# Kernel tuning notes

Measured on AMD Instinct MI355X. Metric: run time of the kernel, lower is better.

Reference implementation:

```python
import jax, jax.numpy as jnp
import numpy as np

D_MODEL = 1024
N_HEADS = 16
D_HEAD = D_MODEL // N_HEADS
D_FF = 4096
BATCH = 2
SEQ = 2048
LN_EPS = 1e-5


def setup_inputs() -> dict:
    key = jax.random.key(0)
    ks = jax.random.split(key, 12)
    s = 1.0 / np.sqrt(D_MODEL)
    x = jax.random.normal(ks[0], (BATCH, SEQ, D_MODEL), dtype=jnp.float32)
    mask = jnp.broadcast_to(jnp.tril(jnp.ones((SEQ, SEQ), jnp.int32)), (BATCH, SEQ, SEQ))
    return {
        "x": x,
        "mask": mask,
        # per-head projections stacked: [H, D, Dh] (bias=False in source)
        "Wq": jax.random.normal(ks[1], (N_HEADS, D_MODEL, D_HEAD), jnp.float32) * s,
        "Wk": jax.random.normal(ks[2], (N_HEADS, D_MODEL, D_HEAD), jnp.float32) * s,
        "Wv": jax.random.normal(ks[3], (N_HEADS, D_MODEL, D_HEAD), jnp.float32) * s,
        "Wo": jax.random.normal(ks[4], (D_MODEL, D_MODEL), jnp.float32) * s,
        "ln1_w": jnp.ones((D_MODEL,), jnp.float32),
        "ln1_b": jnp.zeros((D_MODEL,), jnp.float32),
        "ln2_w": jnp.ones((D_MODEL,), jnp.float32),
        "ln2_b": jnp.zeros((D_MODEL,), jnp.float32),
        "W1": jax.random.normal(ks[5], (D_MODEL, D_FF), jnp.float32) * s,
        "b1": jnp.zeros((D_FF,), jnp.float32),
        "W2": jax.random.normal(ks[6], (D_FF, D_MODEL), jnp.float32) * (1.0 / np.sqrt(D_FF)),
        "b2": jnp.zeros((D_MODEL,), jnp.float32),
    }


def layer_norm(x, w, b):
    mu = jnp.mean(x, axis=-1, keepdims=True)
    var = jnp.var(x, axis=-1, keepdims=True)
    return (x - mu) * jax.lax.rsqrt(var + LN_EPS) * w + b


def reference(x, mask, Wq, Wk, Wv, Wo, ln1_w, ln1_b, ln2_w, ln2_b, W1, b1, W2, b2):
    # pre-LN masked self-attention
    h = layer_norm(x, ln1_w, ln1_b)
    q = jnp.einsum("bsd,hde->bhse", h, Wq)  # [B,H,S,Dh]
    k = jnp.einsum("bsd,hde->bhse", h, Wk)
    v = jnp.einsum("bsd,hde->bhse", h, Wv)
    scores = jnp.einsum("bhse,bhte->bhst", q, k) / np.sqrt(D_HEAD)
    scores = jnp.where(mask[:, None, :, :].astype(bool), scores, -jnp.inf)
    weights = jax.nn.softmax(scores, axis=-1)
    attn = jnp.einsum("bhst,bhte->bhse", weights, v)  # [B,H,S,Dh]
    # concat heads (head order = last-dim order in torch.cat)
    concat = attn.transpose(0, 2, 1, 3).reshape(x.shape[0], x.shape[1], D_MODEL)
    att_out = concat @ Wo
    att_x = x + att_out
    # FFN with exact (erf) GELU, matching nn.GELU default
    h2 = layer_norm(att_x, ln2_w, ln2_b)
    ff = jax.nn.gelu(h2 @ W1 + b1, approximate=False) @ W2 + b2
    return att_x + ff
```

## Files before the change

kernel.cpp:

```cpp
#include <hip/hip_runtime.h>
#include <hip/hip_bf16.h>
#include <math.h>

#define D_MODEL 1024
#define N_HEADS 16
#define D_HEAD  64
#define D_FF    4096
#define BATCH   2
#define SEQ     2048
#define NTOK    (BATCH*SEQ)

typedef __hip_bfloat16 bf16;
typedef __attribute__((ext_vector_type(8))) short short8;
typedef __attribute__((ext_vector_type(4))) float floatx4;

template<typename TIN>
__global__ void ln_kernel(const TIN* __restrict__ x,
                          const float* __restrict__ w,
                          const float* __restrict__ b,
                          bf16* __restrict__ out) {
    int row = blockIdx.x;
    int tid = threadIdx.x;
    const long base = (long)row * D_MODEL;
    float v[4];
    float s = 0.f, sq = 0.f;
#pragma unroll
    for (int i = 0; i < 4; ++i) {
        float xv = (float)x[base + tid + i*256];
        v[i] = xv; s += xv; sq += xv*xv;
    }
    __shared__ float r1[256], r2[256];
    r1[tid] = s; r2[tid] = sq; __syncthreads();
    for (int off = 128; off > 0; off >>= 1) {
        if (tid < off) { r1[tid] += r1[tid+off]; r2[tid] += r2[tid+off]; }
        __syncthreads();
    }
    float mean = r1[0] * (1.f/D_MODEL);
    float var  = r2[0] * (1.f/D_MODEL) - mean*mean;
    float rstd = rsqrtf(var + 1e-5f);
#pragma unroll
    for (int i = 0; i < 4; ++i) {
        int c = tid + i*256;
        out[base + c] = __float2bfloat16((v[i] - mean) * rstd * w[c] + b[c]);
    }
}

__global__ __launch_bounds__(256) void wcvt_kernel(const float* __restrict__ W,
                                                   bf16* __restrict__ Wt,
                                                   int K, int N) {
    __shared__ float t[32][33];
    int n0 = blockIdx.x * 32, k0 = blockIdx.y * 32;
    int lx = threadIdx.x & 31, ly = threadIdx.x >> 5;
#pragma unroll
    for (int i = 0; i < 4; ++i) {
        int k = ly + i * 8;
        t[k][lx] = W[(long)(k0 + k) * N + n0 + lx];
    }
    __syncthreads();
#pragma unroll
    for (int i = 0; i < 4; ++i) {
        int n = ly + i * 8;
        Wt[(long)(n0 + n) * K + k0 + lx] = __float2bfloat16(t[lx][n]);
    }
}

__global__ __launch_bounds__(256) void wcvt_wo_w1(const float* __restrict__ Wo,
                                                  const float* __restrict__ W1,
                                                  bf16* __restrict__ wo_bf,
                                                  bf16* __restrict__ w1_bf) {
    __shared__ float t[32][33];
    int gx = blockIdx.x;
    const float* W; bf16* Wt; int N, n0;
    if (gx < 32) { W = Wo; Wt = wo_bf; N = D_MODEL; n0 = gx * 32; }
    else         { W = W1; Wt = w1_bf; N = D_FF;    n0 = (gx - 32) * 32; }
    int k0 = blockIdx.y * 32;
    int lx = threadIdx.x & 31, ly = threadIdx.x >> 5;
#pragma unroll
    for (int i = 0; i < 4; ++i) {
        int k = ly + i * 8;
        t[k][lx] = W[(long)(k0 + k) * N + n0 + lx];
    }
    __syncthreads();
#pragma unroll
    for (int i = 0; i < 4; ++i) {
        int n = ly + i * 8;
        Wt[(long)(n0 + n) * D_MODEL + k0 + lx] = __float2bfloat16(t[lx][n]);
    }
}

__global__ __launch_bounds__(256) void wcvt_qkv(const float* __restrict__ Wq,
                                                const float* __restrict__ Wk,
                                                const float* __restrict__ Wv,
                                                bf16* __restrict__ outp) {
    __shared__ float t[32][33];
    int z = blockIdx.z, mat = z >> 4, head = z & 15;
    const float* W = (mat == 0 ? Wq : mat == 1 ? Wk : Wv) + (long)head * D_MODEL * D_HEAD;
    bf16* Wt = outp + (long)z * D_HEAD * D_MODEL;
    int n0 = blockIdx.x * 32, k0 = blockIdx.y * 32;
    int lx = threadIdx.x & 31, ly = threadIdx.x >> 5;
#pragma unroll
    for (int i = 0; i < 4; ++i) {
        int k = ly + i * 8;
        t[k][lx] = W[(long)(k0 + k) * D_HEAD + n0 + lx];
    }
    __syncthreads();
#pragma unroll
    for (int i = 0; i < 4; ++i) {
        int n = ly + i * 8;
        Wt[(long)(n0 + n) * D_MODEL + k0 + lx] = __float2bfloat16(t[lx][n]);
    }
}

__device__ inline void swz2d(int& bx, int& by) {
    int gx = gridDim.x;
    int nwg = gx * gridDim.y;
    int bid = blockIdx.y * gx + blockIdx.x;
    int swz = (bid & 7) * (nwg >> 3) + (bid >> 3);
    bx = swz % gx;
    by = swz / gx;
}

template<int ROWS>
__device__ inline void stage_tile(const bf16* g, int gstride, short* lds) {
    int lane = threadIdx.x & 63, wave = threadIdx.x >> 6;
#pragma unroll
    for (int it = 0; it < ROWS / 64; ++it) {
        int c = wave + it * 4;
        const bf16* gp = g + (long)(c * 16 + (lane >> 2)) * gstride + (lane & 3) * 8;
        short* lp = lds + c * 512 + lane * 8;
        __builtin_amdgcn_global_load_lds(
            (const __attribute__((address_space(1))) void*)gp,
            (__attribute__((address_space(3))) void*)lp, 16, 0, 0);
    }
}

template<int BM, int BN, int BK>
__device__ inline void gemm_accum(const bf16* __restrict__ A, int lda,
                                  const bf16* __restrict__ Wt, int K,
                                  int row0, int col0, short* As, short* Bs,
                                  floatx4 (&acc)[BM/32][BN/32]) {
    constexpr int MI  = BM / 32;
    constexpr int NR  = BN / 32;
    constexpr int ASZ = BM * BK;
    constexpr int BSZ = BN * BK;
    int tid  = threadIdx.x;
    int wave = tid >> 6, lane = tid & 63;
    int quad = lane >> 4, l16 = lane & 15;
    int wm = (wave >> 1) * (BM / 2);
    int wn = (wave & 1) * (BN / 2);

    auto stage = [&](int k0, int buf) {
#pragma unroll
        for (int kk = 0; kk < BK; kk += 32) {
            stage_tile<BM>(A  + (long)row0 * lda + k0 + kk, lda,
                           As + buf * ASZ + (kk / 32) * BM * 32);
            stage_tile<BN>(Wt + (long)col0 * K   + k0 + kk, K,
                           Bs + buf * BSZ + (kk / 32) * BN * 32);
        }
    };

    stage(0, 0);
    __syncthreads();

    int cur = 0;
    for (int k0 = 0; k0 < K; k0 += BK) {
        if (k0 + BK < K) stage(k0 + BK, cur ^ 1);

#pragma unroll
        for (int p = 0; p < BK / 32; ++p) {
            const short* Ap = As + cur * ASZ + p * BM * 32;
            const short* Bp = Bs + cur * BSZ + p * BN * 32;
            short8 af[MI], bfr[NR];
#pragma unroll
            for (int mi = 0; mi < MI; ++mi)
                af[mi] = *(const short8*)&Ap[(wm + mi * 16 + l16) * 32 + quad * 8];
#pragma unroll
            for (int ni = 0; ni < NR; ++ni)
                bfr[ni] = *(const short8*)&Bp[(wn + ni * 16 + l16) * 32 + quad * 8];
#pragma unroll
            for (int mi = 0; mi < MI; ++mi)
#pragma unroll
                for (int ni = 0; ni < NR; ++ni)
                    acc[mi][ni] = __builtin_amdgcn_mfma_f32_16x16x32_bf16(
                        af[mi], bfr[ni], acc[mi][ni], 0, 0, 0);
        }
        __syncthreads();
        cur ^= 1;
    }
}

template<int BM, int BN, int BK, int BIAS, int ACT, int RES, int OUTBF16>
__global__ __launch_bounds__(256) void mfma_gemm_bf(
    const bf16* __restrict__ A, int lda,
    const bf16* __restrict__ Wt, int K,
    const float* __restrict__ bias, const float* __restrict__ resid,
    void* __restrict__ Cout, int ldc)
{
    constexpr int MI = BM / 32;
    constexpr int NR = BN / 32;
    __shared__ short As[2 * BM * BK];
    __shared__ short Bs[2 * BN * BK];
    int bx, by; swz2d(bx, by);
    int row0 = by * BM, col0 = bx * BN;
    int tid = threadIdx.x, wave = tid >> 6, lane = tid & 63;
    int quad = lane >> 4, l16 = lane & 15;
    int wm = (wave >> 1) * (BM / 2);
    int wn = (wave & 1) * (BN / 2);

    floatx4 acc[MI][NR];
#pragma unroll
    for (int mi = 0; mi < MI; ++mi)
#pragma unroll
        for (int ni = 0; ni < NR; ++ni)
            acc[mi][ni] = (floatx4){0.f, 0.f, 0.f, 0.f};

    gemm_accum<BM, BN, BK>(A, lda, Wt, K, row0, col0, As, Bs, acc);

#pragma unroll
    for (int mi = 0; mi < MI; ++mi) {
#pragma unroll
        for (int ni = 0; ni < NR; ++ni) {
#pragma unroll
            for (int r = 0; r < 4; ++r) {
                int row = row0 + wm + mi * 16 + quad * 4 + r;
                int col = col0 + wn + ni * 16 + l16;
                float v = acc[mi][ni][r];
                if (BIAS) v += bias[col];
                if (ACT == 1) {
                    float x2 = v * v;
                    float arg = fminf(v * fmaf(0.1029392f, x2, 2.3021182f), 20.f);
                    float t = exp2f(arg);
                    v = v * t * __builtin_amdgcn_rcpf(t + 1.f);
                }
                long idx = (long)row * ldc + col;
                if (RES == 1) v += resid[idx];
                if (OUTBF16) ((bf16*)Cout)[idx] = __float2bfloat16(v);
                else         ((float*)Cout)[idx] = v;
            }
        }
    }
}

struct QkvOut { bf16* o[3]; };

#define RG(buf,mat,kh) (((buf)*4 + (mat)*2 + (kh)) * 8192)
#define G256_BAR  asm volatile("s_barrier" ::: "memory")
#define G256_VM4  asm volatile("s_waitcnt vmcnt(4)" ::: "memory")
#define G256_VM0  asm volatile("s_waitcnt vmcnt(0)" ::: "memory")

__device__ inline void stage2(const bf16* g0, const bf16* g1, int koff, short* lp) {
    __builtin_amdgcn_global_load_lds(
        (const __attribute__((address_space(1))) void*)(g0 + koff),
        (__attribute__((address_space(3))) void*)lp, 16, 0, 0);
    __builtin_amdgcn_global_load_lds(
        (const __attribute__((address_space(1))) void*)(g1 + koff),
        (__attribute__((address_space(3))) void*)(lp + 4096), 16, 0, 0);
}

template<int MH>
__device__ inline void rd_frags(const short* lds, int ra, int rb,
                                int wr, int wc, int l16, int quad,
                                short8 (&areg)[4], short8 (&breg)[4]) {
    if (MH == 0) {
#pragma unroll
        for (int ni = 0; ni < 4; ++ni) {
            int row = wc * 64 + ni * 16 + l16;
            int sl = quad ^ ((row >> 1) & 3);
            breg[ni] = *(const short8*)&lds[rb + row * 32 + sl * 8];
        }
    }
#pragma unroll
    for (int mi = 0; mi < 4; ++mi) {
        int row = wr * 128 + (MH * 4 + mi) * 16 + l16;
        int sl = quad ^ ((row >> 1) & 3);
        areg[mi] = *(const short8*)&lds[ra + row * 32 + sl * 8];
    }
}

template<int MH>
__device__ inline void do_mfma16(const short8 (&areg)[4], const short8 (&breg)[4],
                                 floatx4 (&acc)[8][4]) {
    __builtin_amdgcn_s_setprio(1);
#pragma unroll
    for (int mi = 0; mi < 4; ++mi)
#pragma unroll
        for (int ni = 0; ni < 4; ++ni)
            acc[MH * 4 + mi][ni] = __builtin_amdgcn_mfma_f32_16x16x32_bf16(
                areg[mi], breg[ni], acc[MH * 4 + mi][ni], 0, 0, 0);
    __builtin_amdgcn_s_setprio(0);
}

template<int EPI>
__global__ __launch_bounds__(512, 1) void gemm256_kernel(
    const bf16* __restrict__ A, int lda,
    const bf16* __restrict__ Wt, int ldw, int K,
    const float* __restrict__ bias,
    bf16* __restrict__ Cout, int ldc, QkvOut qa)
{
    __shared__ short lds[65536];
    const int NT = K / 64;
    int row0 = blockIdx.y * 256, col0 = blockIdx.x * 256;
    int tid = threadIdx.x;
    int lane = tid & 63, wave = tid >> 6;
    int quad = lane >> 4, l16 = lane & 15;
    int wr = wave >> 2, wc = wave & 3;

    int srow = tid >> 2, slot = tid & 3;
    int cA0 = slot ^ ((srow >> 1) & 3);
    int cA1 = slot ^ (((srow + 128) >> 1) & 3);
    const bf16* a0 = A  + (long)(row0 + srow) * lda + cA0 * 8;
    const bf16* a1 = A  + (long)(row0 + srow + 128) * lda + cA1 * 8;
    const bf16* b0 = Wt + (long)(col0 + srow) * ldw + cA0 * 8;
    const bf16* b1 = Wt + (long)(col0 + srow + 128) * ldw + cA1 * 8;
    short* lt = lds + tid * 8;

    floatx4 acc[8][4];
#pragma unroll
    for (int mi = 0; mi < 8; ++mi)
#pragma unroll
        for (int ni = 0; ni < 4; ++ni)
            acc[mi][ni] = (floatx4){0.f, 0.f, 0.f, 0.f};

    stage2(a0, a1, 0,  lt + RG(0,0,0));
    stage2(b0, b1, 0,  lt + RG(0,1,0));
    stage2(a0, a1, 32, lt + RG(0,0,1));
    stage2(b0, b1, 32, lt + RG(0,1,1));
    stage2(a0, a1, 64, lt + RG(1,0,0));
    stage2(b0, b1, 64, lt + RG(1,1,0));
    G256_VM4;
    G256_BAR;

    short8 areg[4], breg[4];

    for (int i = 0; i < NT / 2; ++i) {
        int T = 2 * i;
        bool s2 = (T + 2 < NT);
        bool s3 = (T + 3 < NT);
        int k1off = (T + 1) * 64;
        int k2off = (T + 2) * 64;
        int k3off = (T + 3) * 64;

        rd_frags<0>(lds, RG(0,0,0), RG(0,1,0), wr, wc, l16, quad, areg, breg);
        stage2(a0, a1, k1off + 32, lt + RG(1,0,1));
        G256_BAR;
        do_mfma16<0>(areg, breg, acc);
        G256_BAR;

        rd_frags<1>(lds, RG(0,0,0), RG(0,1,0), wr, wc, l16, quad, areg, breg);
        stage2(b0, b1, k1off + 32, lt + RG(1,1,1));
        G256_BAR;
        do_mfma16<1>(areg, breg, acc);
        G256_BAR;

        rd_frags<0>(lds, RG(0,0,1), RG(0,1,1), wr, wc, l16, quad, areg, breg);
        if (s2) stage2(a0, a1, k2off, lt + RG(0,0,0));
        G256_BAR;
        do_mfma16<0>(areg, breg, acc);
        G256_BAR;

        rd_frags<1>(lds, RG(0,0,1), RG(0,1,1), wr, wc, l16, quad, areg, breg);
        if (s2) stage2(b0, b1, k2off, lt + RG(0,1,0));
        G256_BAR;
        do_mfma16<1>(areg, breg, acc);
        if (s2) { G256_VM4; } else { G256_VM0; }
        G256_BAR;

        rd_frags<0>(lds, RG(1,0,0), RG(1,1,0), wr, wc, l16, quad, areg, breg);
        if (s2) stage2(a0, a1, k2off + 32, lt + RG(0,0,1));
        G256_BAR;
        do_mfma16<0>(areg, breg, acc);
        G256_BAR;

        rd_frags<1>(lds, RG(1,0,0), RG(1,1,0), wr, wc, l16, quad, areg, breg);
        if (s2) stage2(b0, b1, k2off + 32, lt + RG(0,1,1));
        G256_BAR;
        do_mfma16<1>(areg, breg, acc);
        G256_BAR;

        rd_frags<0>(lds, RG(1,0,1), RG(1,1,1), wr, wc, l16, quad, areg, breg);
        if (s3) stage2(a0, a1, k3off, lt + RG(1,0,0));
        G256_BAR;
        do_mfma16<0>(areg, breg, acc);
        G256_BAR;

        rd_frags<1>(lds, RG(1,0,1), RG(1,1,1), wr, wc, l16, quad, areg, breg);
        if (s3) stage2(b0, b1, k3off, lt + RG(1,1,0));
        G256_BAR;
        do_mfma16<1>(areg, breg, acc);
        if (s3) { G256_VM4; } else { G256_VM0; }
        G256_BAR;
    }

#pragma unroll
    for (int mi = 0; mi < 8; ++mi) {
#pragma unroll
        for (int ni = 0; ni < 4; ++ni) {
#pragma unroll
            for (int r = 0; r < 4; ++r) {
                int row = row0 + wr * 128 + mi * 16 + quad * 4 + r;
                int col = col0 + wc * 64 + ni * 16 + l16;
                float v = acc[mi][ni][r];
                if constexpr (EPI == 0) {
                    v += bias[col];
                    float x2 = v * v;
                    float arg = fminf(v * fmaf(0.1029392f, x2, 2.3021182f), 20.f);
                    float t = exp2f(arg);
                    v = v * t * __builtin_amdgcn_rcpf(t + 1.f);
                    Cout[(long)row * ldc + col] = __float2bfloat16(v);
                } else {
                    int mat = col >> 10, hd = (col >> 6) & 15, d = col & 63;
                    int b = row >> 11, s = row & 2047;
                    qa.o[mat][(((long)(b * 16 + hd) * SEQ + s) << 6) + d] =
                        __float2bfloat16(v);
                }
            }
        }
    }
}

__global__ __launch_bounds__(256) void fattn_mfma(const bf16* __restrict__ q,
                                                  const bf16* __restrict__ k,
                                                  const bf16* __restrict__ v,
                                                  bf16* __restrict__ po,
                                                  float* __restrict__ lz) {
    int byr = blockIdx.y;
    int tile = (byr < 8) ? byr : 23 - byr;
    int chunk = blockIdx.z;
    int bh = blockIdx.x;
    int tid = threadIdx.x;
    int wave = tid >> 6, lane = tid & 63;
    int quad = lane >> 4, l16 = lane & 15;
    const long base = (long)bh * SEQ * D_HEAD;
    const int r0g = tile * 128;

    bf16*  pob = po + (long)chunk * 32 * SEQ * 64;
    float* lzb = lz + (long)chunk * 32 * SEQ;

    __shared__ short Ks[64 * 72];
    __shared__ short Vt[64 * 72];
    __shared__ short Ps[4][32 * 72];

    short8 qf[2][2];
#pragma unroll
    for (int rb = 0; rb < 2; ++rb) {
        const short* qrow = (const short*)(q + base +
            (long)(r0g + wave * 32 + rb * 16 + l16) * D_HEAD);
        qf[rb][0] = *(const short8*)(qrow + quad * 8);
        qf[rb][1] = *(const short8*)(qrow + 32 + quad * 8);
#pragma unroll
        for (int c = 0; c < 2; ++c)
#pragma unroll
            for (int j = 0; j < 8; ++j) {
                float f = __uint_as_float(((unsigned)(unsigned short)qf[rb][c][j]) << 16)
                          * 0.18033688f;
                qf[rb][c][j] = __builtin_bit_cast(short, __float2bfloat16(f));
            }
    }

    short8 onesf;
    {
        short o1 = (l16 == 0) ? (short)0x3F80 : (short)0;
#pragma unroll
        for (int j = 0; j < 8; ++j) onesf[j] = o1;
    }

    floatx4 o[2][4];
#pragma unroll
    for (int rb = 0; rb < 2; ++rb)
#pragma unroll
        for (int nb = 0; nb < 4; ++nb) o[rb][nb] = (floatx4){0.f, 0.f, 0.f, 0.f};
    floatx4 l4[2] = {(floatx4){0.f,0.f,0.f,0.f}, (floatx4){0.f,0.f,0.f,0.f}};

    const int kt0 = chunk ? tile + 1 : 0;
    const int kt1 = chunk ? 2 * tile + 1 : tile;
    for (int kt = kt0; kt <= kt1; ++kt) {
        __syncthreads();
        {
            int t = tid >> 2, c = tid & 3;
            const short* krow = (const short*)(k + base + (long)(kt * 64 + t) * D_HEAD);
            *(uint4*)&Ks[t * 72 + c * 16]     = *(const uint4*)(krow + c * 16);
            *(uint4*)&Ks[t * 72 + c * 16 + 8] = *(const uint4*)(krow + c * 16 + 8);
        }
        {
            int tp = (tid & 31) * 2;
            int d0 = ((tid >> 5) & 7) * 8;
            const short* v0 = (const short*)(v + base + (long)(kt * 64 + tp) * D_HEAD + d0);
            short va[8], vb[8];
            *(uint4*)va = *(const uint4*)v0;
            *(uint4*)vb = *(const uint4*)(v0 + D_HEAD);
#pragma unroll
            for (int j = 0; j < 8; ++j) {
                unsigned pk = (unsigned)(unsigned short)va[j] |
                              ((unsigned)(unsigned short)vb[j] << 16);
                *(unsigned*)&Vt[(d0 + j) * 72 + tp] = pk;
            }
        }
        __syncthreads();

        if (kt * 64 > r0g + wave * 32 + 31) continue;

        floatx4 s[2][4];
#pragma unroll
        for (int nb = 0; nb < 4; ++nb) {
            short8 kf0 = *(const short8*)&Ks[(nb * 16 + l16) * 72 + quad * 8];
            short8 kf1 = *(const short8*)&Ks[(nb * 16 + l16) * 72 + 32 + quad * 8];
#pragma unroll
            for (int rb = 0; rb < 2; ++rb) {
                floatx4 z4 = (floatx4){0.f, 0.f, 0.f, 0.f};
                z4 = __builtin_amdgcn_mfma_f32_16x16x32_bf16(qf[rb][0], kf0, z4, 0, 0, 0);
                z4 = __builtin_amdgcn_mfma_f32_16x16x32_bf16(qf[rb][1], kf1, z4, 0, 0, 0);
                s[rb][nb] = z4;
            }
        }

        if (kt >= 2 * tile) {
#pragma unroll
            for (int rb = 0; rb < 2; ++rb) {
                int qg = r0g + wave * 32 + rb * 16 + quad * 4;
#pragma unroll
                for (int nb = 0; nb < 4; ++nb) {
                    int kg = kt * 64 + nb * 16 + l16;
#pragma unroll
                    for (int r = 0; r < 4; ++r)
                        if (kg > qg + r) s[rb][nb][r] = -1e30f;
                }
            }
        }

        short* Pw = &Ps[wave][0];
#pragma unroll
        for (int rb = 0; rb < 2; ++rb)
#pragma unroll
            for (int nb = 0; nb < 4; ++nb)
#pragma unroll
                for (int r = 0; r < 4; ++r) {
                    float p = exp2f(s[rb][nb][r]);
                    Pw[(rb * 16 + quad * 4 + r) * 72 + nb * 16 + l16] =
                        __builtin_bit_cast(short, __float2bfloat16(p));
                }

        short8 pf[2][2];
#pragma unroll
        for (int rb = 0; rb < 2; ++rb) {
            pf[rb][0] = *(const short8*)&Pw[(rb * 16 + l16) * 72 + quad * 8];
            pf[rb][1] = *(const short8*)&Pw[(rb * 16 + l16) * 72 + 32 + quad * 8];
        }
#pragma unroll
        for (int nb = 0; nb < 4; ++nb) {
            short8 vf0 = *(const short8*)&Vt[(nb * 16 + l16) * 72 + quad * 8];
            short8 vf1 = *(const short8*)&Vt[(nb * 16 + l16) * 72 + 32 + quad * 8];
#pragma unroll
            for (int rb = 0; rb < 2; ++rb) {
                o[rb][nb] = __builtin_amdgcn_mfma_f32_16x16x32_bf16(pf[rb][0], vf0, o[rb][nb], 0, 0, 0);
                o[rb][nb] = __builtin_amdgcn_mfma_f32_16x16x32_bf16(pf[rb][1], vf1, o[rb][nb], 0, 0, 0);
            }
        }
#pragma unroll
        for (int rb = 0; rb < 2; ++rb) {
            l4[rb] = __builtin_amdgcn_mfma_f32_16x16x32_bf16(pf[rb][0], onesf, l4[rb], 0, 0, 0);
            l4[rb] = __builtin_amdgcn_mfma_f32_16x16x32_bf16(pf[rb][1], onesf, l4[rb], 0, 0, 0);
        }
    }

#pragma unroll
    for (int rb = 0; rb < 2; ++rb) {
#pragma unroll
        for (int nb = 0; nb < 4; ++nb)
#pragma unroll
            for (int r = 0; r < 4; ++r) {
                int row = r0g + wave * 32 + rb * 16 + quad * 4 + r;
                pob[((long)bh * SEQ + row) * 64 + nb * 16 + l16] =
                    __float2bfloat16(o[rb][nb][r]);
            }
        if (l16 == 0) {
#pragma unroll
            for (int r = 0; r < 4; ++r) {
                int row = r0g + wave * 32 + rb * 16 + quad * 4 + r;
                lzb[(long)bh * SEQ + row] = l4[rb][r];
            }
        }
    }
}

__global__ __launch_bounds__(256) void attn_combine(const bf16* __restrict__ po,
                                                    const float* __restrict__ lz,
                                                    bf16* __restrict__ cc) {
    const long CH = 32L * SEQ * 64;
    int row = blockIdx.x;
    int b = row >> 11, s = row & 2047;
    int tid = threadIdx.x;
    int col = tid * 4;
    int h = col >> 6, d = col & 63;
    long pidx = ((long)(b * 16 + h) * SEQ + s) * 64 + d;
    uint2 u0 = *(const uint2*)((const unsigned short*)po + pidx);
    uint2 u1 = *(const uint2*)((const unsigned short*)po + CH + pidx);
    long li = (long)(b * 16 + h) * SEQ + s;
    float linv = 1.f / (lz[li] + lz[32L * SEQ + li]);
    unsigned ua[4] = {u0.x & 0xFFFFu, u0.x >> 16, u0.y & 0xFFFFu, u0.y >> 16};
    unsigned ub[4] = {u1.x & 0xFFFFu, u1.x >> 16, u1.y & 0xFFFFu, u1.y >> 16};
    unsigned short rr[4];
#pragma unroll
    for (int i = 0; i < 4; ++i) {
        float ov = __uint_as_float(ua[i] << 16) + __uint_as_float(ub[i] << 16);
        rr[i] = __builtin_bit_cast(unsigned short, __float2bfloat16(ov * linv));
    }
    uint2 w;
    w.x = (unsigned)rr[0] | ((unsigned)rr[1] << 16);
    w.y = (unsigned)rr[2] | ((unsigned)rr[3] << 16);
    *(uint2*)((unsigned short*)cc + (long)row * D_MODEL + col) = w;
}

extern "C" void kernel_launch(void* const* d_in, const int* in_sizes, int n_in,
                              void* d_out, int out_size, void* d_ws, size_t ws_size,
                              hipStream_t stream) {
    const float* x    = (const float*)d_in[0];
    const float* Wq   = (const float*)d_in[2];
    const float* Wk   = (const float*)d_in[3];
    const float* Wv   = (const float*)d_in[4];
    const float* Wo   = (const float*)d_in[5];
    const float* ln1w = (const float*)d_in[6];
    const float* ln1b = (const float*)d_in[7];
    const float* ln2w = (const float*)d_in[8];
    const float* ln2b = (const float*)d_in[9];
    const float* W1   = (const float*)d_in[10];
    const float* b1   = (const float*)d_in[11];
    const float* W2   = (const float*)d_in[12];
    const float* b2   = (const float*)d_in[13];
    float* out = (float*)d_out;

    char* wsb = (char*)d_ws;
    const size_t MB = 1024*1024;
    bf16*  h1      = (bf16*)(wsb + 0*MB);
    bf16*  qb      = (bf16*)(wsb + 8*MB);
    bf16*  kb      = (bf16*)(wsb + 16*MB);
    bf16*  vb      = (bf16*)(wsb + 24*MB);
    bf16*  wqkv_bf = (bf16*)(wsb + 32*MB);
    bf16*  po      = (bf16*)(wsb + 32*MB);
    float* lz      = (float*)(wsb + 48*MB);
    bf16*  cc      = (bf16*)(wsb + 0*MB);
    bf16*  wo_bf   = (bf16*)(wsb + 8*MB);
    bf16*  w1_bf   = (bf16*)(wsb + 10*MB);
    bf16*  h2      = (bf16*)(wsb + 0*MB);
    bf16*  ff      = (bf16*)(wsb + 24*MB);
    bf16*  w2_bf   = (bf16*)(wsb + 8*MB);

    QkvOut qa; qa.o[0] = qb; qa.o[1] = kb; qa.o[2] = vb;

    ln_kernel<float><<<NTOK, 256, 0, stream>>>(x, ln1w, ln1b, h1);

    wcvt_qkv<<<dim3(2, 32, 48), 256, 0, stream>>>(Wq, Wk, Wv, wqkv_bf);

    gemm256_kernel<1><<<dim3(12, 16), 512, 0, stream>>>(
        h1, D_MODEL, wqkv_bf, D_MODEL, D_MODEL, nullptr, nullptr, 0, qa);

    fattn_mfma<<<dim3(BATCH*N_HEADS, SEQ/128, 2), 256, 0, stream>>>(qb, kb, vb, po, lz);

    attn_combine<<<NTOK, 256, 0, stream>>>(po, lz, cc);

    wcvt_wo_w1<<<dim3(160, 32), 256, 0, stream>>>(Wo, W1, wo_bf, w1_bf);

    mfma_gemm_bf<64,256,64,0,0,1,0><<<dim3(4,64), 256, 0, stream>>>(
        cc, D_MODEL, wo_bf, D_MODEL, nullptr, x, out, D_MODEL);

    ln_kernel<float><<<NTOK, 256, 0, stream>>>(out, ln2w, ln2b, h2);

    QkvOut qdummy = {};
    gemm256_kernel<0><<<dim3(16, 16), 512, 0, stream>>>(
        h2, D_MODEL, w1_bf, D_MODEL, D_MODEL, b1, ff, D_FF, qdummy);

    wcvt_kernel<<<dim3(D_MODEL/32, D_FF/32), 256, 0, stream>>>(W2, w2_bf, D_FF, D_MODEL);

    mfma_gemm_bf<64,256,64,1,0,1,0><<<dim3(4,64), 256, 0, stream>>>(
        ff, D_FF, w2_bf, D_FF, b2, out, out, D_MODEL);
}
```

Measured before the change: 394.3 us.

## Hand-schedule LDS fragment reads, swizzle GEMM blocks, shrink Wo/W2 tiles

The 256x256 GEMM now reads its LDS fragments with inline ds_read_b128 assembly using precomputed per-lane offsets, then waits on lgkmcnt before each MFMA block under a scheduling barrier. Block indices are remapped through a 2D swizzle, presumably to improve L2 locality. The Wo and W2 projection GEMMs drop from 64x256 to 64x128 tiles, doubling the grid to fill more CUs. These changes aim to cut address arithmetic and compiler-inserted waits, improve cache reuse, and raise occupancy. In exchange they give less data reuse per tile and an explicit full wait that may serialize LDS reads with the MFMAs.

Result: faster. 373.5 us (-5.3%).

```diff
diff --git a/kernel.cpp b/kernel.cpp
--- a/kernel.cpp
+++ b/kernel.cpp
@@ -247,6 +247,8 @@
 #define G256_BAR  asm volatile("s_barrier" ::: "memory")
 #define G256_VM4  asm volatile("s_waitcnt vmcnt(4)" ::: "memory")
 #define G256_VM0  asm volatile("s_waitcnt vmcnt(0)" ::: "memory")
+#define G256_LGKM0 do { asm volatile("s_waitcnt lgkmcnt(0)" ::: "memory"); \
+                        __builtin_amdgcn_sched_barrier(0); } while (0)
 
 __device__ inline void stage2(const bf16* g0, const bf16* g1, int koff, short* lp) {
     __builtin_amdgcn_global_load_lds(
@@ -258,22 +260,20 @@
 }
 
 template<int MH>
-__device__ inline void rd_frags(const short* lds, int ra, int rb,
-                                int wr, int wc, int l16, int quad,
-                                short8 (&areg)[4], short8 (&breg)[4]) {
+__device__ inline void rd_frags_asm(unsigned ldsbase, int ra, int rb,
+                                    const unsigned (&aoff)[8], const unsigned (&boff)[4],
+                                    short8 (&areg)[4], short8 (&breg)[4]) {
     if (MH == 0) {
 #pragma unroll
         for (int ni = 0; ni < 4; ++ni) {
-            int row = wc * 64 + ni * 16 + l16;
-            int sl = quad ^ ((row >> 1) & 3);
-            breg[ni] = *(const short8*)&lds[rb + row * 32 + sl * 8];
+            unsigned ad = ldsbase + (unsigned)(rb * 2) + boff[ni];
+            asm volatile("ds_read_b128 %0, %1" : "=v"(breg[ni]) : "v"(ad));
         }
     }
 #pragma unroll
     for (int mi = 0; mi < 4; ++mi) {
-        int row = wr * 128 + (MH * 4 + mi) * 16 + l16;
-        int sl = quad ^ ((row >> 1) & 3);
-        areg[mi] = *(const short8*)&lds[ra + row * 32 + sl * 8];
+        unsigned ad = ldsbase + (unsigned)(ra * 2) + aoff[MH * 4 + mi];
+        asm volatile("ds_read_b128 %0, %1" : "=v"(areg[mi]) : "v"(ad));
     }
 }
 
@@ -299,7 +299,8 @@
 {
     __shared__ short lds[65536];
     const int NT = K / 64;
-    int row0 = blockIdx.y * 256, col0 = blockIdx.x * 256;
+    int bx, by; swz2d(bx, by);
+    int row0 = by * 256, col0 = bx * 256;
     int tid = threadIdx.x;
     int lane = tid & 63, wave = tid >> 6;
     int quad = lane >> 4, l16 = lane & 15;
@@ -314,6 +315,21 @@
     const bf16* b1 = Wt + (long)(col0 + srow + 128) * ldw + cA1 * 8;
     short* lt = lds + tid * 8;
 
+    unsigned ldsbase = (unsigned)(unsigned long long)(void*)&lds[0];
+    unsigned aoff[8], boff[4];
+#pragma unroll
+    for (int mi = 0; mi < 8; ++mi) {
+        int row = wr * 128 + mi * 16 + l16;
+        int sl = quad ^ ((row >> 1) & 3);
+        aoff[mi] = (unsigned)((row * 32 + sl * 8) * 2);
+    }
+#pragma unroll
+    for (int ni = 0; ni < 4; ++ni) {
+        int row = wc * 64 + ni * 16 + l16;
+        int sl = quad ^ ((row >> 1) & 3);
+        boff[ni] = (unsigned)((row * 32 + sl * 8) * 2);
+    }
+
     floatx4 acc[8][4];
 #pragma unroll
     for (int mi = 0; mi < 8; ++mi)
@@ -340,52 +356,60 @@
         int k2off = (T + 2) * 64;
         int k3off = (T + 3) * 64;
 
-        rd_frags<0>(lds, RG(0,0,0), RG(0,1,0), wr, wc, l16, quad, areg, breg);
+        rd_frags_asm<0>(ldsbase, RG(0,0,0), RG(0,1,0), aoff, boff, areg, breg);
         stage2(a0, a1, k1off + 32, lt + RG(1,0,1));
         G256_BAR;
+        G256_LGKM0;
         do_mfma16<0>(areg, breg, acc);
         G256_BAR;
 
-        rd_frags<1>(lds, RG(0,0,0), RG(0,1,0), wr, wc, l16, quad, areg, breg);
+        rd_frags_asm<1>(ldsbase, RG(0,0,0), RG(0,1,0), aoff, boff, areg, breg);
         stage2(b0, b1, k1off + 32, lt + RG(1,1,1));
         G256_BAR;
+        G256_LGKM0;
         do_mfma16<1>(areg, breg, acc);
         G256_BAR;
 
-        rd_frags<0>(lds, RG(0,0,1), RG(0,1,1), wr, wc, l16, quad, areg, breg);
+        rd_frags_asm<0>(ldsbase, RG(0,0,1), RG(0,1,1), aoff, boff, areg, breg);
         if (s2) stage2(a0, a1, k2off, lt + RG(0,0,0));
         G256_BAR;
+        G256_LGKM0;
         do_mfma16<0>(areg, breg, acc);
         G256_BAR;
 
-        rd_frags<1>(lds, RG(0,0,1), RG(0,1,1), wr, wc, l16, quad, areg, breg);
+        rd_frags_asm<1>(ldsbase, RG(0,0,1), RG(0,1,1), aoff, boff, areg, breg);
         if (s2) stage2(b0, b1, k2off, lt + RG(0,1,0));
         G256_BAR;
+        G256_LGKM0;
         do_mfma16<1>(areg, breg, acc);
         if (s2) { G256_VM4; } else { G256_VM0; }
         G256_BAR;
 
-        rd_frags<0>(lds, RG(1,0,0), RG(1,1,0), wr, wc, l16, quad, areg, breg);
+        rd_frags_asm<0>(ldsbase, RG(1,0,0), RG(1,1,0), aoff, boff, areg, breg);
         if (s2) stage2(a0, a1, k2off + 32, lt + RG(0,0,1));
         G256_BAR;
+        G256_LGKM0;
         do_mfma16<0>(areg, breg, acc);
         G256_BAR;
 
-        rd_frags<1>(lds, RG(1,0,0), RG(1,1,0), wr, wc, l16, quad, areg, breg);
+        rd_frags_asm<1>(ldsbase, RG(1,0,0), RG(1,1,0), aoff, boff, areg, breg);
         if (s2) stage2(b0, b1, k2off + 32, lt + RG(0,1,1));
         G256_BAR;
+        G256_LGKM0;
         do_mfma16<1>(areg, breg, acc);
         G256_BAR;
 
-        rd_frags<0>(lds, RG(1,0,1), RG(1,1,1), wr, wc, l16, quad, areg, breg);
+        rd_frags_asm<0>(ldsbase, RG(1,0,1), RG(1,1,1), aoff, boff, areg, breg);
         if (s3) stage2(a0, a1, k3off, lt + RG(1,0,0));
         G256_BAR;
+        G256_LGKM0;
         do_mfma16<0>(areg, breg, acc);
         G256_BAR;
 
-        rd_frags<1>(lds, RG(1,0,1), RG(1,1,1), wr, wc, l16, quad, areg, breg);
+        rd_frags_asm<1>(ldsbase, RG(1,0,1), RG(1,1,1), aoff, boff, areg, breg);
         if (s3) stage2(b0, b1, k3off, lt + RG(1,1,0));
         G256_BAR;
+        G256_LGKM0;
         do_mfma16<1>(areg, breg, acc);
         if (s3) { G256_VM4; } else { G256_VM0; }
         G256_BAR;
@@ -645,6 +669,7 @@
     bf16*  w2_bf   = (bf16*)(wsb + 8*MB);
 
     QkvOut qa; qa.o[0] = qb; qa.o[1] = kb; qa.o[2] = vb;
+    QkvOut qdummy = {};
 
     ln_kernel<float><<<NTOK, 256, 0, stream>>>(x, ln1w, ln1b, h1);
 
@@ -659,17 +684,16 @@
 
     wcvt_wo_w1<<<dim3(160, 32), 256, 0, stream>>>(Wo, W1, wo_bf, w1_bf);
 
-    mfma_gemm_bf<64,256,64,0,0,1,0><<<dim3(4,64), 256, 0, stream>>>(
+    mfma_gemm_bf<64,128,64,0,0,1,0><<<dim3(8,64), 256, 0, stream>>>(
         cc, D_MODEL, wo_bf, D_MODEL, nullptr, x, out, D_MODEL);
 
     ln_kernel<float><<<NTOK, 256, 0, stream>>>(out, ln2w, ln2b, h2);
 
-    QkvOut qdummy = {};
     gemm256_kernel<0><<<dim3(16, 16), 512, 0, stream>>>(
         h2, D_MODEL, w1_bf, D_MODEL, D_MODEL, b1, ff, D_FF, qdummy);
 
     wcvt_kernel<<<dim3(D_MODEL/32, D_FF/32), 256, 0, stream>>>(W2, w2_bf, D_FF, D_MODEL);
 
-    mfma_gemm_bf<64,256,64,1,0,1,0><<<dim3(4,64), 256, 0, stream>>>(
+    mfma_gemm_bf<64,128,64,1,0,1,0><<<dim3(8,64), 256, 0, stream>>>(
         ff, D_FF, w2_bf, D_FF, b2, out, out, D_MODEL);
 }
```
